# Kernel tuning notes

Measured on AMD Instinct MI355X. Metric: run time of the kernel, lower is better.

Reference implementation:

```python
import jax, jax.numpy as jnp
import numpy as np

B, L, N, H = 4, 8192, 16, 64
BASE = 10000.0
N_SEG = 16  # packed segments per row, each of length L // N_SEG


def setup_inputs() -> dict:
    key = jax.random.key(0)
    x = jax.random.normal(key, (B, L, N, H), dtype=jnp.float32)
    # index_tensor: lengths of packed sub-sequences at the front of each row,
    # zeros elsewhere (matches the module's docstring convention). Sum == L.
    seg_len = L // N_SEG
    idx = np.zeros((B, L), dtype=np.int64)
    idx[:, :N_SEG] = seg_len
    return {"x": x, "index_tensor": jnp.asarray(idx)}


def _positions(index_tensor, L):
    """Segment-reset positions: concat of arange(l) for each length l, zero-padded.

    Zero-length entries contribute empty aranges, so filtering nonzeros (as the
    torch code does) is equivalent to cumulative-sum bookkeeping over raw lengths.
    """
    def row(lengths):
        csum = jnp.cumsum(lengths)          # inclusive cumsum of segment lengths
        starts = csum - lengths             # exclusive cumsum = segment start offsets
        j = jnp.arange(L)
        seg = jnp.clip(jnp.searchsorted(csum, j, side='right'), 0, L - 1)
        return jnp.where(j < csum[-1], j - starts[seg], 0)
    return jax.vmap(row)(index_tensor).astype(jnp.float32)  # [B, L]


def reference(x, index_tensor):
    Bx, Lx, n, h = x.shape
    inv_freq = 1.0 / BASE ** (jnp.arange(0, h, 2, dtype=jnp.float32) / h)  # [h/2]
    pos = _positions(index_tensor, Lx)                    # [B, L]
    freqs = pos[..., None] * inv_freq                     # [B, L, h/2]
    emb = jnp.concatenate([freqs, freqs], axis=-1)        # [B, L, h]
    cos = jnp.cos(emb)[:, :, None, :]                     # [B, L, 1, h]
    sin = jnp.sin(emb)[:, :, None, :]
    x1, x2 = jnp.split(x, 2, axis=-1)
    rot = jnp.concatenate([-x2, x1], axis=-1)             # rotate_half
    return x * cos + rot * sin
```

## Files before the change

### kernel.cpp

```cpp
#include <hip/hip_runtime.h>
#include <cmath>

#define B_ 4
#define L_ 8192
#define N_ 16
#define H_ 64

typedef float f32x4 __attribute__((ext_vector_type(4)));

__global__ __launch_bounds__(1024)
void pos_kernel(const long long* __restrict__ idx, float* __restrict__ pos) {
    __shared__ int csum[L_];
    __shared__ int wp[17];
    const int b   = blockIdx.x;
    const int tid = threadIdx.x;
    constexpr int CHUNK = L_ / 1024;

    const long long* row = idx + (size_t)b * L_;

    int local[CHUNK];
    int s = 0;
#pragma unroll
    for (int i = 0; i < CHUNK; ++i) {
        s += (int)row[tid * CHUNK + i];
        local[i] = s;
    }

    const int lane = tid & 63, wv = tid >> 6;
    int scan = s;
#pragma unroll
    for (int off = 1; off < 64; off <<= 1) {
        int n = __shfl_up(scan, off);
        if (lane >= off) scan += n;
    }
    if (lane == 63) wp[wv + 1] = scan;
    if (tid == 0)   wp[0] = 0;
    __syncthreads();
    if (tid == 0) {
        int a = 0;
        for (int i = 1; i <= 16; ++i) { a += wp[i]; wp[i] = a; }
    }
    __syncthreads();

    const int off0 = wp[wv] + (scan - s);
#pragma unroll
    for (int i = 0; i < CHUNK; ++i) csum[tid * CHUNK + i] = off0 + local[i];
    __syncthreads();

    const int total = csum[L_ - 1];

    int p[CHUNK];
#pragma unroll
    for (int u = 0; u < CHUNK; ++u) p[u] = 0;
#pragma unroll
    for (int k = L_ / 2; k > 0; k >>= 1) {
#pragma unroll
        for (int u = 0; u < CHUNK; ++u) {
            const int j = tid + u * 1024;
            p[u] += (csum[p[u] + k - 1] <= j) ? k : 0;
        }
    }
#pragma unroll
    for (int u = 0; u < CHUNK; ++u) {
        const int j    = tid + u * 1024;
        const int excl = p[u] ? csum[p[u] - 1] : 0;
        pos[(size_t)b * L_ + j] = (j < total) ? (float)(j - excl) : 0.f;
    }
}

__global__ __launch_bounds__(256)
void rope_kernel(const float* __restrict__ x,
                 const float* __restrict__ pos,
                 float* __restrict__ out) {
    constexpr int NTHR  = 524288;
    constexpr int ITERS = (B_ * L_ * N_ * H_ / 4) / NTHR;

    const int t  = blockIdx.x * 256 + threadIdx.x;
    const int qp = t & 15;
    const float sgn = (qp < 8) ? -1.f : 1.f;

    constexpr float NEG_LN_BASE_OVER_32 = -0.28782313662425f;
    constexpr float INV_2PI             = 0.15915493667126f;
    float f[4];
#pragma unroll
    for (int j = 0; j < 4; ++j)
        f[j] = __expf((float)((qp & 7) * 4 + j) * NEG_LN_BASE_OVER_32) * INV_2PI;

#pragma unroll 4
    for (int i = 0; i < ITERS; ++i) {
        const size_t v  = (size_t)t + (size_t)i * NTHR;
        const size_t bl = v >> 8;
        const float  p  = pos[bl];

        const f32x4 a = __builtin_nontemporal_load((const f32x4*)(x) + v);

        f32x4 pr;
#pragma unroll
        for (int j = 0; j < 4; ++j) pr[j] = __shfl_xor(a[j], 8);

        f32x4 o;
#pragma unroll
        for (int j = 0; j < 4; ++j) {
            float ph = p * f[j];
            ph -= floorf(ph);
            const float cv = __builtin_amdgcn_cosf(ph);
            const float sv = __builtin_amdgcn_sinf(ph);
            o[j] = a[j] * cv + sgn * pr[j] * sv;
        }

        __builtin_nontemporal_store(o, (f32x4*)(out) + v);
    }
}

extern "C" void kernel_launch(void* const* d_in, const int* in_sizes, int n_in,
                              void* d_out, int out_size, void* d_ws, size_t ws_size,
                              hipStream_t stream) {
    const float*     x   = (const float*)d_in[0];
    const long long* idx = (const long long*)d_in[1];
    float*           out = (float*)d_out;
    float*           pos = (float*)d_ws;

    pos_kernel<<<B_, 1024, 0, stream>>>(idx, pos);
    rope_kernel<<<2048, 256, 0, stream>>>(x, pos, out);
}
```

Baseline: 60.33 us.

## Assign one (b,l) row per wave and reuse sin/cos across heads

Remaps the rope kernel so each 64-lane wave owns one (batch, position) row and walks four head groups of that row. Each thread computes cos/sin once and reuses them for its four loads, instead of recomputing the transcendentals on every iteration. All four loads are issued before any compute to raise memory-level parallelism. The grid grows fourfold and each thread does a fixed small amount of work, which adds block scheduling overhead and gives less latency hiding per thread.

Result: faster. 52.63 us (-12.8%).

```diff
diff --git a/kernel.cpp b/kernel.cpp
--- a/kernel.cpp
+++ b/kernel.cpp
@@ -72,43 +72,43 @@
 void rope_kernel(const float* __restrict__ x,
                  const float* __restrict__ pos,
                  float* __restrict__ out) {
-    constexpr int NTHR  = 524288;
-    constexpr int ITERS = (B_ * L_ * N_ * H_ / 4) / NTHR;
+    const int    t    = blockIdx.x * 256 + threadIdx.x;
+    const int    lane = threadIdx.x & 63;
+    const int    qp   = lane & 15;
+    const size_t bl   = (size_t)t >> 6;
+    const size_t base = bl * 256 + (size_t)lane;
 
-    const int t  = blockIdx.x * 256 + threadIdx.x;
-    const int qp = t & 15;
-    const float sgn = (qp < 8) ? -1.f : 1.f;
+    const float p = pos[bl];
 
     constexpr float NEG_LN_BASE_OVER_32 = -0.28782313662425f;
     constexpr float INV_2PI             = 0.15915493667126f;
-    float f[4];
+    const float sgn = (qp < 8) ? -1.f : 1.f;
+
+    float cv[4], ssv[4];
 #pragma unroll
-    for (int j = 0; j < 4; ++j)
-        f[j] = __expf((float)((qp & 7) * 4 + j) * NEG_LN_BASE_OVER_32) * INV_2PI;
+    for (int j = 0; j < 4; ++j) {
+        const float f = __expf((float)((qp & 7) * 4 + j) * NEG_LN_BASE_OVER_32)
+                        * INV_2PI;
+        float ph = p * f;
+        ph -= floorf(ph);
+        cv[j]  = __builtin_amdgcn_cosf(ph);
+        ssv[j] = sgn * __builtin_amdgcn_sinf(ph);
+    }
 
-#pragma unroll 4
-    for (int i = 0; i < ITERS; ++i) {
-        const size_t v  = (size_t)t + (size_t)i * NTHR;
-        const size_t bl = v >> 8;
-        const float  p  = pos[bl];
+    f32x4 a[4];
+#pragma unroll
+    for (int i = 0; i < 4; ++i)
+        a[i] = __builtin_nontemporal_load((const f32x4*)(x) + base + (size_t)(i * 64));
 
-        const f32x4 a = __builtin_nontemporal_load((const f32x4*)(x) + v);
-
+#pragma unroll
+    for (int i = 0; i < 4; ++i) {
         f32x4 pr;
 #pragma unroll
-        for (int j = 0; j < 4; ++j) pr[j] = __shfl_xor(a[j], 8);
-
+        for (int j = 0; j < 4; ++j) pr[j] = __shfl_xor(a[i][j], 8);
         f32x4 o;
 #pragma unroll
-        for (int j = 0; j < 4; ++j) {
-            float ph = p * f[j];
-            ph -= floorf(ph);
-            const float cv = __builtin_amdgcn_cosf(ph);
-            const float sv = __builtin_amdgcn_sinf(ph);
-            o[j] = a[j] * cv + sgn * pr[j] * sv;
-        }
-
-        __builtin_nontemporal_store(o, (f32x4*)(out) + v);
+        for (int j = 0; j < 4; ++j) o[j] = a[i][j] * cv[j] + pr[j] * ssv[j];
+        __builtin_nontemporal_store(o, (f32x4*)(out) + base + (size_t)(i * 64));
     }
 }
 
@@ -121,5 +121,6 @@
     float*           pos = (float*)d_ws;
 
     pos_kernel<<<B_, 1024, 0, stream>>>(idx, pos);
-    rope_kernel<<<2048, 256, 0, stream>>>(x, pos, out);
+
+    rope_kernel<<<8192, 256, 0, stream>>>(x, pos, out);
 }
```
